# Kernel optimization log

Measured on AMD Instinct MI355X. Metric: run time of the kernel, lower is better.

The kernel has to match this reference:

```python
import jax, jax.numpy as jnp
import numpy as np

N_HEADS = 8
N_GROUPS = 8  # n_channels=256 > 64
COLOR_WEIGHT = 1.2
EPS = 1e-5


def setup_inputs() -> dict:
    key = jax.random.key(0)
    ks = jax.random.split(key, 6)
    B, C, H, W = 16, 256, 32, 32
    x = jax.random.normal(ks[0], (B, C, H, W), dtype=jnp.float32)
    std = 0.02
    wq = jax.random.normal(ks[1], (C, C), dtype=jnp.float32) * std
    wk = jax.random.normal(ks[2], (C, C), dtype=jnp.float32) * std
    wv = jax.random.normal(ks[3], (C, C), dtype=jnp.float32) * std
    wo = jax.random.normal(ks[4], (C, C), dtype=jnp.float32) * std
    bq = jnp.zeros((C,), jnp.float32)
    bk = jnp.zeros((C,), jnp.float32)
    bv = jnp.zeros((C,), jnp.float32)
    bo = jnp.zeros((C,), jnp.float32)
    gn_w = jnp.ones((C,), jnp.float32)
    gn_b = jnp.zeros((C,), jnp.float32)
    return {"x": x, "wq": wq, "bq": bq, "wk": wk, "bk": bk,
            "wv": wv, "bv": bv, "wo": wo, "bo": bo,
            "gn_w": gn_w, "gn_b": gn_b}


def reference(x, wq, bq, wk, bk, wv, bv, wo, bo, gn_w, gn_b):
    B, C, H, W = x.shape
    S = H * W
    nh = N_HEADS
    hd = C // nh
    scale = hd ** (-0.5)

    # GroupNorm over (channels_per_group, spatial) per sample
    xf = x.reshape(B, C, S)
    xg = xf.reshape(B, N_GROUPS, (C // N_GROUPS) * S)
    mean = xg.mean(axis=-1, keepdims=True)
    var = xg.var(axis=-1, keepdims=True)
    xn = ((xg - mean) * jax.lax.rsqrt(var + EPS)).reshape(B, C, S)
    xn = xn * gn_w[None, :, None] + gn_b[None, :, None]

    xt = jnp.swapaxes(xn, 1, 2)  # [B, S, C]
    q = xt @ wq.T + bq
    k = xt @ wk.T + bk
    v = xt @ wv.T + bv
    # [B, S, C] -> [B, nh, S, hd]
    q = q.reshape(B, S, nh, hd).transpose(0, 2, 1, 3)
    k = k.reshape(B, S, nh, hd).transpose(0, 2, 1, 3)
    v = v.reshape(B, S, nh, hd).transpose(0, 2, 1, 3)

    attn = jnp.einsum('bhid,bhjd->bhij', q, k) * scale  # [B, nh, S, S]
    # color bias (is_grayscale=False path): k.transpose(-2,-1).reshape(B,nh,S,hd)
    k_color = jnp.swapaxes(k, -2, -1).reshape(B, nh, S, hd)
    color_attn = jnp.abs(q - k_color).mean(axis=-1, keepdims=True)  # [B,nh,S,1]
    attn = attn + COLOR_WEIGHT * color_attn
    attn = jax.nn.softmax(attn, axis=-1)
    # dropout is inference no-op

    out = jnp.einsum('bhij,bhjd->bhid', attn, v)  # [B, nh, S, hd]
    out = out.transpose(0, 2, 1, 3).reshape(B, S, C)
    out = out @ wo.T + bo
    out = jnp.swapaxes(out, 1, 2).reshape(B, C, H, W)
    return out
```

## Files before the change

kernel.cpp:

```cpp
#include <hip/hip_runtime.h>


typedef __attribute__((ext_vector_type(8))) short bf16x8;
typedef __attribute__((ext_vector_type(4))) float f32x4;

static __device__ __forceinline__ unsigned cvt_pk(float lo, float hi) {
  unsigned r;
  asm("v_cvt_pk_bf16_f32 %0, %1, %2" : "=v"(r) : "v"(lo), "v"(hi));
  return r;
}

__global__ __launch_bounds__(256) void prep_kernel(
    const float* __restrict__ x, float2* __restrict__ statsp,
    const float* __restrict__ w0, const float* __restrict__ w1,
    const float* __restrict__ w2, const float* __restrict__ w3,
    short* __restrict__ o0, short* __restrict__ o1,
    short* __restrict__ o2, short* __restrict__ o3) {
  int tid = threadIdx.x;
  if (blockIdx.x < 512) {
    __shared__ float red[8];
    int bg = blockIdx.x >> 2, qtr = blockIdx.x & 3;
    const float4* x4 = (const float4*)(x + (size_t)bg * 32 * 1024);
    float s = 0.f, ss = 0.f;
#pragma unroll
    for (int p = 0; p < 8; ++p) {
      float4 vv = x4[qtr * 2048 + p * 256 + tid];
      s += (vv.x + vv.y) + (vv.z + vv.w);
      ss += vv.x * vv.x + vv.y * vv.y + vv.z * vv.z + vv.w * vv.w;
    }
#pragma unroll
    for (int o = 32; o > 0; o >>= 1) {
      s += __shfl_down(s, o);
      ss += __shfl_down(ss, o);
    }
    if ((tid & 63) == 0) { red[tid >> 6] = s; red[4 + (tid >> 6)] = ss; }
    __syncthreads();
    if (tid == 0) {
      float S = (red[0] + red[1]) + (red[2] + red[3]);
      float SS = (red[4] + red[5]) + (red[6] + red[7]);
      statsp[bg * 4 + qtr] = make_float2(S, SS);
    }
  } else {
    int idx = blockIdx.x - 512;
    int sel = idx >> 5, blk = idx & 31;
    const float* src = sel == 0 ? w0 : sel == 1 ? w1 : sel == 2 ? w2 : w3;
    short* dst = sel == 0 ? o0 : sel == 1 ? o1 : sel == 2 ? o2 : o3;
    int i = (blk * 256 + tid) * 8;
    float4 a = *(const float4*)(src + i);
    float4 b = *(const float4*)(src + i + 4);
    uint4 r;
    r.x = cvt_pk(a.x, a.y);
    r.y = cvt_pk(a.z, a.w);
    r.z = cvt_pk(b.x, b.y);
    r.w = cvt_pk(b.z, b.w);
    *(uint4*)(dst + i) = r;
  }
}

static __device__ __forceinline__ float2 combine_stats(const float2* __restrict__ sp,
                                                       int bgidx) {
  float2 p0 = sp[bgidx * 4 + 0];
  float2 p1 = sp[bgidx * 4 + 1];
  float2 p2 = sp[bgidx * 4 + 2];
  float2 p3 = sp[bgidx * 4 + 3];
  float S = (p0.x + p1.x) + (p2.x + p3.x);
  float SS = (p0.y + p1.y) + (p2.y + p3.y);
  float mean = S * (1.f / 32768.f);
  float var = SS * (1.f / 32768.f) - mean * mean;
  return make_float2(mean, rsqrtf(var + 1e-5f));
}

__global__ __launch_bounds__(256, 4) void qkv_mfma(
    const float* __restrict__ x, const float2* __restrict__ statsp,
    const float* __restrict__ gnw, const float* __restrict__ gnb,
    const short* __restrict__ Wq, const short* __restrict__ Wk,
    const short* __restrict__ Wv,
    const float* __restrict__ bq, const float* __restrict__ bk,
    const float* __restrict__ bv, short* __restrict__ outq,
    short* __restrict__ outk, short* __restrict__ outvt, float scaleq) {
  __shared__ __align__(16) char smem[20480];
  short* As = (short*)smem;
  int tid = threadIdx.x;
  int m0 = blockIdx.x * 64, n0 = blockIdx.y * 64;
  int w = tid >> 6, lane = tid & 63, g = lane >> 4, c = lane & 15;
  int wm = w >> 1, wn = w & 1;
  int srow = tid >> 2, sk = (tid & 3) * 8;
  int bsmp = m0 >> 10, s0 = m0 & 1023;
  int c2 = tid & 15, sg = tid >> 4;
  const float4* xb = (const float4*)(x + (size_t)(bsmp * 256) * 1024);
  unsigned* A32 = (unsigned*)As;
  f32x4 accq[2][2], acck[2][2], accv[2][2];
#pragma unroll
  for (int i = 0; i < 2; ++i)
#pragma unroll
    for (int j = 0; j < 2; ++j) {
      accq[i][j] = (f32x4){0.f, 0.f, 0.f, 0.f};
      acck[i][j] = (f32x4){0.f, 0.f, 0.f, 0.f};
      accv[i][j] = (f32x4){0.f, 0.f, 0.f, 0.f};
    }
  float a0, a1, b0v, b1v;
  float4 u, v;
  bf16x8 wqr, wkr, wvr;
  {
    float2 st = combine_stats(statsp, bsmp * 8);
    int ch0 = c2 * 2;
    a0 = gnw[ch0] * st.y; b0v = gnb[ch0] - st.x * a0;
    a1 = gnw[ch0 + 1] * st.y; b1v = gnb[ch0 + 1] - st.x * a1;
    u = xb[(size_t)ch0 * 256 + (s0 >> 2) + sg];
    v = xb[(size_t)(ch0 + 1) * 256 + (s0 >> 2) + sg];
    wqr = *(const bf16x8*)(Wq + (size_t)(n0 + srow) * 256 + sk);
    wkr = *(const bf16x8*)(Wk + (size_t)(n0 + srow) * 256 + sk);
    wvr = *(const bf16x8*)(Wv + (size_t)(n0 + srow) * 256 + sk);
  }
  for (int kb = 0; kb < 8; ++kb) {
    {
      int r0 = (sg * 4) * 20 + c2;
      A32[r0]      = cvt_pk(u.x * a0 + b0v, v.x * a1 + b1v);
      A32[r0 + 20] = cvt_pk(u.y * a0 + b0v, v.y * a1 + b1v);
      A32[r0 + 40] = cvt_pk(u.z * a0 + b0v, v.z * a1 + b1v);
      A32[r0 + 60] = cvt_pk(u.w * a0 + b0v, v.w * a1 + b1v);
    }
    *(bf16x8*)(As + 2560 + srow * 40 + sk) = wqr;
    *(bf16x8*)(As + 5120 + srow * 40 + sk) = wkr;
    *(bf16x8*)(As + 7680 + srow * 40 + sk) = wvr;
    __syncthreads();
    if (kb < 7) {
      float2 st = combine_stats(statsp, bsmp * 8 + kb + 1);
      int chn = (kb + 1) * 32 + c2 * 2;
      a0 = gnw[chn] * st.y; b0v = gnb[chn] - st.x * a0;
      a1 = gnw[chn + 1] * st.y; b1v = gnb[chn + 1] - st.x * a1;
      u = xb[(size_t)chn * 256 + (s0 >> 2) + sg];
      v = xb[(size_t)(chn + 1) * 256 + (s0 >> 2) + sg];
      wqr = *(const bf16x8*)(Wq + (size_t)(n0 + srow) * 256 + (kb + 1) * 32 + sk);
      wkr = *(const bf16x8*)(Wk + (size_t)(n0 + srow) * 256 + (kb + 1) * 32 + sk);
      wvr = *(const bf16x8*)(Wv + (size_t)(n0 + srow) * 256 + (kb + 1) * 32 + sk);
    }
    bf16x8 af[2], wfq[2], wfk[2], wfv[2];
#pragma unroll
    for (int i = 0; i < 2; ++i)
      af[i] = *(const bf16x8*)(As + (wm * 32 + i * 16 + c) * 40 + g * 8);
#pragma unroll
    for (int j = 0; j < 2; ++j) {
      int rr = (wn * 32 + j * 16 + c) * 40 + g * 8;
      wfq[j] = *(const bf16x8*)(As + 2560 + rr);
      wfk[j] = *(const bf16x8*)(As + 5120 + rr);
      wfv[j] = *(const bf16x8*)(As + 7680 + rr);
    }
#pragma unroll
    for (int i = 0; i < 2; ++i)
#pragma unroll
      for (int j = 0; j < 2; ++j) {
        accq[i][j] = __builtin_amdgcn_mfma_f32_16x16x32_bf16(wfq[j], af[i], accq[i][j], 0, 0, 0);
        acck[i][j] = __builtin_amdgcn_mfma_f32_16x16x32_bf16(wfk[j], af[i], acck[i][j], 0, 0, 0);
        accv[i][j] = __builtin_amdgcn_mfma_f32_16x16x32_bf16(af[i], wfv[j], accv[i][j], 0, 0, 0);
      }
    __syncthreads();
  }
  short* Tb = (short*)smem;
  int mrd = tid >> 2, ncol = (tid & 3) * 16;
#pragma unroll
  for (int i = 0; i < 2; ++i)
#pragma unroll
    for (int j = 0; j < 2; ++j) {
      float4 b4 = *(const float4*)&bq[n0 + wn * 32 + j * 16 + 4 * g];
      float v0 = (accq[i][j][0] + b4.x) * scaleq;
      float v1 = (accq[i][j][1] + b4.y) * scaleq;
      float v2 = (accq[i][j][2] + b4.z) * scaleq;
      float v3 = (accq[i][j][3] + b4.w) * scaleq;
      *(uint2*)(Tb + (wm * 32 + i * 16 + c) * 72 + wn * 32 + j * 16 + 4 * g) =
          make_uint2(cvt_pk(v0, v1), cvt_pk(v2, v3));
    }
  __syncthreads();
  {
    bf16x8 r0 = *(const bf16x8*)(Tb + mrd * 72 + ncol);
    bf16x8 r1 = *(const bf16x8*)(Tb + mrd * 72 + ncol + 8);
    short* dst = outq + (size_t)(m0 + mrd) * 256 + n0 + ncol;
    *(bf16x8*)dst = r0;
    *(bf16x8*)(dst + 8) = r1;
  }
  __syncthreads();
#pragma unroll
  for (int i = 0; i < 2; ++i)
#pragma unroll
    for (int j = 0; j < 2; ++j) {
      float4 b4 = *(const float4*)&bk[n0 + wn * 32 + j * 16 + 4 * g];
      float v0 = acck[i][j][0] + b4.x;
      float v1 = acck[i][j][1] + b4.y;
      float v2 = acck[i][j][2] + b4.z;
      float v3 = acck[i][j][3] + b4.w;
      *(uint2*)(Tb + (wm * 32 + i * 16 + c) * 72 + wn * 32 + j * 16 + 4 * g) =
          make_uint2(cvt_pk(v0, v1), cvt_pk(v2, v3));
    }
  __syncthreads();
  {
    bf16x8 r0 = *(const bf16x8*)(Tb + mrd * 72 + ncol);
    bf16x8 r1 = *(const bf16x8*)(Tb + mrd * 72 + ncol + 8);
    short* dst = outk + (size_t)(m0 + mrd) * 256 + n0 + ncol;
    *(bf16x8*)dst = r0;
    *(bf16x8*)(dst + 8) = r1;
  }
  __syncthreads();
#pragma unroll
  for (int i = 0; i < 2; ++i)
#pragma unroll
    for (int j = 0; j < 2; ++j) {
      float bvv = bv[n0 + wn * 32 + j * 16 + c];
      float v0 = accv[i][j][0] + bvv;
      float v1 = accv[i][j][1] + bvv;
      float v2 = accv[i][j][2] + bvv;
      float v3 = accv[i][j][3] + bvv;
      *(uint2*)(Tb + (wn * 32 + j * 16 + c) * 72 + wm * 32 + i * 16 + 4 * g) =
          make_uint2(cvt_pk(v0, v1), cvt_pk(v2, v3));
    }
  __syncthreads();
  {
    bf16x8 r0 = *(const bf16x8*)(Tb + mrd * 72 + ncol);
    bf16x8 r1 = *(const bf16x8*)(Tb + mrd * 72 + ncol + 8);
    short* dst = outvt + (size_t)(bsmp * 256 + n0 + mrd) * 1024 + s0 + ncol;
    *(bf16x8*)dst = r0;
    *(bf16x8*)(dst + 8) = r1;
  }
}

#define KSTR 40
#define VSTR 72
#define PSTR 72

__global__ __launch_bounds__(256, 4) void flash_mfma(
    const short* __restrict__ q, const short* __restrict__ k,
    const short* __restrict__ vt, short* __restrict__ out) {
  __shared__ short Ks[2][64 * KSTR];
  __shared__ short Vts[2][32 * VSTR];
  __shared__ short Ps[4 * 32 * PSTR];
  int id = blockIdx.x;
  int swz = (id & 7) * 128 + (id >> 3);
  int bh = swz >> 3, qt = swz & 7;
  int b = bh >> 3, h = bh & 7;
  int tid = threadIdx.x;
  int w = tid >> 6, lane = tid & 63, g = lane >> 4, c = lane & 15;
  short* Psw = Ps + w * 32 * PSTR;
  const size_t qrow0 = (size_t)b * 1024 + qt * 128 + w * 32;
  const int hoff = h * 32;
  bf16x8 aq[2];
#pragma unroll
  for (int mt = 0; mt < 2; ++mt)
    aq[mt] = *(const bf16x8*)(q + (qrow0 + mt * 16 + c) * 256 + hoff + g * 8);
  bf16x8 ones;
#pragma unroll
  for (int i = 0; i < 8; ++i) ones[i] = (short)0x3F80;
  f32x4 o_acc[2][2], accl[2];
#pragma unroll
  for (int mt = 0; mt < 2; ++mt) {
    accl[mt] = (f32x4){0.f, 0.f, 0.f, 0.f};
#pragma unroll
    for (int nt = 0; nt < 2; ++nt) o_acc[mt][nt] = (f32x4){0.f, 0.f, 0.f, 0.f};
  }
  const int kr = tid >> 2, kch = (tid & 3) * 8;
  const int vr = tid >> 3, vch = (tid & 7) * 8;
  const short* kbase = k + ((size_t)b * 1024) * 256 + hoff;
  const short* vbase = vt + (((size_t)b * 8 + h) * 32) * 1024;
  {
    bf16x8 k0 = *(const bf16x8*)(kbase + (size_t)kr * 256 + kch);
    bf16x8 v0 = *(const bf16x8*)(vbase + (size_t)vr * 1024 + vch);
    *(bf16x8*)(&Ks[0][kr * KSTR + kch]) = k0;
    *(bf16x8*)(&Vts[0][vr * VSTR + vch]) = v0;
  }
  __syncthreads();
  int cur = 0;
#pragma unroll 2
  for (int t = 0; t < 16; ++t) {
    bf16x8 kN, vN;
    if (t < 15) {
      kN = *(const bf16x8*)(kbase + (size_t)((t + 1) * 64 + kr) * 256 + kch);
      vN = *(const bf16x8*)(vbase + (size_t)vr * 1024 + (t + 1) * 64 + vch);
    }
    bf16x8 bk4[4];
#pragma unroll
    for (int kt = 0; kt < 4; ++kt)
      bk4[kt] = *(const bf16x8*)(&Ks[cur][(kt * 16 + c) * KSTR + g * 8]);
    f32x4 sc[2][4];
    __builtin_amdgcn_s_setprio(1);
#pragma unroll
    for (int mt = 0; mt < 2; ++mt)
#pragma unroll
      for (int kt = 0; kt < 4; ++kt)
        sc[mt][kt] = __builtin_amdgcn_mfma_f32_16x16x32_bf16(
            bk4[kt], aq[mt], (f32x4){0.f, 0.f, 0.f, 0.f}, 0, 0, 0);
    __builtin_amdgcn_s_setprio(0);
#pragma unroll
    for (int mt = 0; mt < 2; ++mt)
#pragma unroll
      for (int kt = 0; kt < 4; ++kt) {
        float p0 = __builtin_amdgcn_exp2f(sc[mt][kt][0]);
        float p1 = __builtin_amdgcn_exp2f(sc[mt][kt][1]);
        float p2 = __builtin_amdgcn_exp2f(sc[mt][kt][2]);
        float p3 = __builtin_amdgcn_exp2f(sc[mt][kt][3]);
        *(uint2*)(Psw + (mt * 16 + c) * PSTR + kt * 16 + 4 * g) =
            make_uint2(cvt_pk(p0, p1), cvt_pk(p2, p3));
      }
#pragma unroll
    for (int jt = 0; jt < 2; ++jt) {
      bf16x8 av[2], bp[2];
#pragma unroll
      for (int nt = 0; nt < 2; ++nt)
        av[nt] = *(const bf16x8*)(&Vts[cur][(nt * 16 + c) * VSTR + jt * 32 + g * 8]);
#pragma unroll
      for (int mt = 0; mt < 2; ++mt)
        bp[mt] = *(const bf16x8*)(Psw + (mt * 16 + c) * PSTR + jt * 32 + g * 8);
      __builtin_amdgcn_s_setprio(1);
#pragma unroll
      for (int mt = 0; mt < 2; ++mt) {
#pragma unroll
        for (int nt = 0; nt < 2; ++nt)
          o_acc[mt][nt] = __builtin_amdgcn_mfma_f32_16x16x32_bf16(
              av[nt], bp[mt], o_acc[mt][nt], 0, 0, 0);
        accl[mt] = __builtin_amdgcn_mfma_f32_16x16x32_bf16(ones, bp[mt], accl[mt], 0, 0, 0);
      }
      __builtin_amdgcn_s_setprio(0);
    }
    if (t < 15) {
      *(bf16x8*)(&Ks[cur ^ 1][kr * KSTR + kch]) = kN;
      *(bf16x8*)(&Vts[cur ^ 1][vr * VSTR + vch]) = vN;
      __syncthreads();
      cur ^= 1;
    }
  }
#pragma unroll
  for (int mt = 0; mt < 2; ++mt) {
    float linv = 1.0f / accl[mt][0];
#pragma unroll
    for (int nt = 0; nt < 2; ++nt) {
      float v0 = o_acc[mt][nt][0] * linv;
      float v1 = o_acc[mt][nt][1] * linv;
      float v2 = o_acc[mt][nt][2] * linv;
      float v3 = o_acc[mt][nt][3] * linv;
      *(uint2*)(out + (qrow0 + mt * 16 + c) * 256 + hoff + nt * 16 + 4 * g) =
          make_uint2(cvt_pk(v0, v1), cvt_pk(v2, v3));
    }
  }
}

__global__ __launch_bounds__(256) void gemm_out(
    const short* __restrict__ A, const short* __restrict__ W,
    const float* __restrict__ bias, float* __restrict__ out) {
  __shared__ __align__(16) char smem[10240];
  short* As = (short*)smem;
  short* Ws = (short*)(smem + 5120);
  int tid = threadIdx.x;
  int m0 = blockIdx.x * 64, n0 = blockIdx.y * 64;
  int w = tid >> 6, lane = tid & 63, g = lane >> 4, c = lane & 15;
  int wm = w >> 1, wn = w & 1;
  int srow = tid >> 2, sk = (tid & 3) * 8;
  f32x4 acc[2][2];
#pragma unroll
  for (int i = 0; i < 2; ++i)
#pragma unroll
    for (int j = 0; j < 2; ++j) acc[i][j] = (f32x4){0.f, 0.f, 0.f, 0.f};
  bf16x8 aR = *(const bf16x8*)(A + (size_t)(m0 + srow) * 256 + sk);
  bf16x8 wR = *(const bf16x8*)(W + (size_t)(n0 + srow) * 256 + sk);
  for (int kb = 0; kb < 8; ++kb) {
    *(bf16x8*)(As + srow * 40 + sk) = aR;
    *(bf16x8*)(Ws + srow * 40 + sk) = wR;
    __syncthreads();
    if (kb < 7) {
      aR = *(const bf16x8*)(A + (size_t)(m0 + srow) * 256 + (kb + 1) * 32 + sk);
      wR = *(const bf16x8*)(W + (size_t)(n0 + srow) * 256 + (kb + 1) * 32 + sk);
    }
    bf16x8 af[2], wf[2];
#pragma unroll
    for (int i = 0; i < 2; ++i)
      af[i] = *(const bf16x8*)(As + (wm * 32 + i * 16 + c) * 40 + g * 8);
#pragma unroll
    for (int j = 0; j < 2; ++j)
      wf[j] = *(const bf16x8*)(Ws + (wn * 32 + j * 16 + c) * 40 + g * 8);
#pragma unroll
    for (int i = 0; i < 2; ++i)
#pragma unroll
      for (int j = 0; j < 2; ++j)
        acc[i][j] = __builtin_amdgcn_mfma_f32_16x16x32_bf16(af[i], wf[j], acc[i][j], 0, 0, 0);
    __syncthreads();
  }
  int bsmp = m0 >> 10, s0 = m0 & 1023;
  float* Tf = (float*)smem;
  for (int half = 0; half < 2; ++half) {
    __syncthreads();
    if (wn == half) {
#pragma unroll
      for (int j = 0; j < 2; ++j) {
        float bvh = bias[n0 + half * 32 + j * 16 + c];
        int nl = j * 16 + c;
#pragma unroll
        for (int i = 0; i < 2; ++i)
#pragma unroll
          for (int r = 0; r < 4; ++r)
            Tf[nl * 68 + ((wm * 32 + i * 16 + 4 * g + r) ^ ((nl & 7) << 2))] =
                acc[i][j][r] + bvh;
      }
    }
    __syncthreads();
    int n = tid >> 3, mc = (tid & 7) * 8;
    float4 v0 = *(const float4*)(Tf + n * 68 + ((mc + 0) ^ ((n & 7) << 2)));
    float4 v1 = *(const float4*)(Tf + n * 68 + ((mc + 4) ^ ((n & 7) << 2)));
    float* dst = out + ((size_t)(bsmp * 256) + n0 + half * 32 + n) * 1024 + s0 + mc;
    *(float4*)dst = v0;
    *(float4*)(dst + 4) = v1;
  }
}

extern "C" void kernel_launch(void* const* d_in, const int* in_sizes, int n_in,
                              void* d_out, int out_size, void* d_ws, size_t ws_size,
                              hipStream_t stream) {
  const float* x   = (const float*)d_in[0];
  const float* wq  = (const float*)d_in[1];
  const float* bq  = (const float*)d_in[2];
  const float* wk  = (const float*)d_in[3];
  const float* bk  = (const float*)d_in[4];
  const float* wv  = (const float*)d_in[5];
  const float* bv  = (const float*)d_in[6];
  const float* wo  = (const float*)d_in[7];
  const float* bo  = (const float*)d_in[8];
  const float* gnw = (const float*)d_in[9];
  const float* gnb = (const float*)d_in[10];
  float* out = (float*)d_out;

  const size_t NE = (size_t)16 * 1024 * 256;
  short* sw  = (short*)d_ws;
  float2* statsp = (float2*)sw;
  short* qb  = sw + NE;
  short* kb  = sw + 2 * NE;
  short* vtb = sw + 3 * NE;
  short* ao  = sw + 4 * NE;
  short* wqb = sw + 5 * NE;
  short* wkb = wqb + 65536;
  short* wvb = wkb + 65536;
  short* wob = wvb + 65536;

  const float SCALE_Q = (float)(0.17677669529663689 * 1.4426950408889634);
  dim3 blk(256);
  prep_kernel<<<dim3(640), blk, 0, stream>>>(x, statsp, wq, wk, wv, wo,
                                             wqb, wkb, wvb, wob);
  qkv_mfma<<<dim3(256, 4), blk, 0, stream>>>(x, statsp, gnw, gnb, wqb, wkb, wvb,
                                             bq, bk, bv, qb, kb, vtb, SCALE_Q);
  flash_mfma<<<dim3(1024), blk, 0, stream>>>(qb, kb, vtb, ao);
  gemm_out<<<dim3(256, 4), blk, 0, stream>>>(ao, wob, bo, out);
}
```

Before: 73.93 us.

## Halve QKV GEMM M-tile to 32 rows and drop register prefetch

The QKV projection kernel now uses 32x64 output tiles instead of 64x64, doubling the grid to 512x4 blocks. Each wave owns a 16-column slice and issues fewer MFMAs per step. The register-level prefetch of the next K-slice is replaced by direct load-then-store each iteration, and launch bounds are raised to 6 blocks per CU. The aim is more parallelism and lower register pressure to hide latency, at the cost of reloading the weight tiles twice as often and losing the software overlap of global loads with MFMA.

```diff
diff --git a/kernel.cpp b/kernel.cpp
--- a/kernel.cpp
+++ b/kernel.cpp
@@ -70,7 +70,7 @@
   return make_float2(mean, rsqrtf(var + 1e-5f));
 }
 
-__global__ __launch_bounds__(256, 4) void qkv_mfma(
+__global__ __launch_bounds__(256, 6) void qkv_mfma(
     const float* __restrict__ x, const float2* __restrict__ statsp,
     const float* __restrict__ gnw, const float* __restrict__ gnb,
     const short* __restrict__ Wq, const short* __restrict__ Wk,
@@ -78,147 +78,113 @@
     const float* __restrict__ bq, const float* __restrict__ bk,
     const float* __restrict__ bv, short* __restrict__ outq,
     short* __restrict__ outk, short* __restrict__ outvt, float scaleq) {
-  __shared__ __align__(16) char smem[20480];
+  __shared__ __align__(16) char smem[17920];
   short* As = (short*)smem;
   int tid = threadIdx.x;
-  int m0 = blockIdx.x * 64, n0 = blockIdx.y * 64;
+  int m0 = blockIdx.x * 32, n0 = blockIdx.y * 64;
   int w = tid >> 6, lane = tid & 63, g = lane >> 4, c = lane & 15;
-  int wm = w >> 1, wn = w & 1;
   int srow = tid >> 2, sk = (tid & 3) * 8;
   int bsmp = m0 >> 10, s0 = m0 & 1023;
   int c2 = tid & 15, sg = tid >> 4;
   const float4* xb = (const float4*)(x + (size_t)(bsmp * 256) * 1024);
   unsigned* A32 = (unsigned*)As;
-  f32x4 accq[2][2], acck[2][2], accv[2][2];
-#pragma unroll
-  for (int i = 0; i < 2; ++i)
-#pragma unroll
-    for (int j = 0; j < 2; ++j) {
-      accq[i][j] = (f32x4){0.f, 0.f, 0.f, 0.f};
-      acck[i][j] = (f32x4){0.f, 0.f, 0.f, 0.f};
-      accv[i][j] = (f32x4){0.f, 0.f, 0.f, 0.f};
-    }
-  float a0, a1, b0v, b1v;
-  float4 u, v;
-  bf16x8 wqr, wkr, wvr;
-  {
-    float2 st = combine_stats(statsp, bsmp * 8);
-    int ch0 = c2 * 2;
-    a0 = gnw[ch0] * st.y; b0v = gnb[ch0] - st.x * a0;
-    a1 = gnw[ch0 + 1] * st.y; b1v = gnb[ch0 + 1] - st.x * a1;
-    u = xb[(size_t)ch0 * 256 + (s0 >> 2) + sg];
-    v = xb[(size_t)(ch0 + 1) * 256 + (s0 >> 2) + sg];
-    wqr = *(const bf16x8*)(Wq + (size_t)(n0 + srow) * 256 + sk);
-    wkr = *(const bf16x8*)(Wk + (size_t)(n0 + srow) * 256 + sk);
-    wvr = *(const bf16x8*)(Wv + (size_t)(n0 + srow) * 256 + sk);
+  f32x4 accq[2], acck[2], accv[2];
+#pragma unroll
+  for (int i = 0; i < 2; ++i) {
+    accq[i] = (f32x4){0.f, 0.f, 0.f, 0.f};
+    acck[i] = (f32x4){0.f, 0.f, 0.f, 0.f};
+    accv[i] = (f32x4){0.f, 0.f, 0.f, 0.f};
   }
   for (int kb = 0; kb < 8; ++kb) {
-    {
+    __syncthreads();
+    if (sg < 8) {
+      float2 st = combine_stats(statsp, bsmp * 8 + kb);
+      int ch0 = kb * 32 + c2 * 2;
+      float a0 = gnw[ch0] * st.y, b0v = gnb[ch0] - st.x * a0;
+      float a1 = gnw[ch0 + 1] * st.y, b1v = gnb[ch0 + 1] - st.x * a1;
+      float4 u = xb[(size_t)ch0 * 256 + (s0 >> 2) + sg];
+      float4 v = xb[(size_t)(ch0 + 1) * 256 + (s0 >> 2) + sg];
       int r0 = (sg * 4) * 20 + c2;
       A32[r0]      = cvt_pk(u.x * a0 + b0v, v.x * a1 + b1v);
       A32[r0 + 20] = cvt_pk(u.y * a0 + b0v, v.y * a1 + b1v);
       A32[r0 + 40] = cvt_pk(u.z * a0 + b0v, v.z * a1 + b1v);
       A32[r0 + 60] = cvt_pk(u.w * a0 + b0v, v.w * a1 + b1v);
     }
-    *(bf16x8*)(As + 2560 + srow * 40 + sk) = wqr;
-    *(bf16x8*)(As + 5120 + srow * 40 + sk) = wkr;
-    *(bf16x8*)(As + 7680 + srow * 40 + sk) = wvr;
-    __syncthreads();
-    if (kb < 7) {
-      float2 st = combine_stats(statsp, bsmp * 8 + kb + 1);
-      int chn = (kb + 1) * 32 + c2 * 2;
-      a0 = gnw[chn] * st.y; b0v = gnb[chn] - st.x * a0;
-      a1 = gnw[chn + 1] * st.y; b1v = gnb[chn + 1] - st.x * a1;
-      u = xb[(size_t)chn * 256 + (s0 >> 2) + sg];
-      v = xb[(size_t)(chn + 1) * 256 + (s0 >> 2) + sg];
-      wqr = *(const bf16x8*)(Wq + (size_t)(n0 + srow) * 256 + (kb + 1) * 32 + sk);
-      wkr = *(const bf16x8*)(Wk + (size_t)(n0 + srow) * 256 + (kb + 1) * 32 + sk);
-      wvr = *(const bf16x8*)(Wv + (size_t)(n0 + srow) * 256 + (kb + 1) * 32 + sk);
-    }
-    bf16x8 af[2], wfq[2], wfk[2], wfv[2];
+    *(bf16x8*)(As + 1280 + srow * 40 + sk) =
+        *(const bf16x8*)(Wq + (size_t)(n0 + srow) * 256 + kb * 32 + sk);
+    *(bf16x8*)(As + 3840 + srow * 40 + sk) =
+        *(const bf16x8*)(Wk + (size_t)(n0 + srow) * 256 + kb * 32 + sk);
+    *(bf16x8*)(As + 6400 + srow * 40 + sk) =
+        *(const bf16x8*)(Wv + (size_t)(n0 + srow) * 256 + kb * 32 + sk);
+    __syncthreads();
+    bf16x8 af[2], wfq, wfk, wfv;
 #pragma unroll
     for (int i = 0; i < 2; ++i)
-      af[i] = *(const bf16x8*)(As + (wm * 32 + i * 16 + c) * 40 + g * 8);
-#pragma unroll
-    for (int j = 0; j < 2; ++j) {
-      int rr = (wn * 32 + j * 16 + c) * 40 + g * 8;
-      wfq[j] = *(const bf16x8*)(As + 2560 + rr);
-      wfk[j] = *(const bf16x8*)(As + 5120 + rr);
-      wfv[j] = *(const bf16x8*)(As + 7680 + rr);
-    }
-#pragma unroll
-    for (int i = 0; i < 2; ++i)
-#pragma unroll
-      for (int j = 0; j < 2; ++j) {
-        accq[i][j] = __builtin_amdgcn_mfma_f32_16x16x32_bf16(wfq[j], af[i], accq[i][j], 0, 0, 0);
-        acck[i][j] = __builtin_amdgcn_mfma_f32_16x16x32_bf16(wfk[j], af[i], acck[i][j], 0, 0, 0);
-        accv[i][j] = __builtin_amdgcn_mfma_f32_16x16x32_bf16(af[i], wfv[j], accv[i][j], 0, 0, 0);
-      }
-    __syncthreads();
-  }
+      af[i] = *(const bf16x8*)(As + (i * 16 + c) * 40 + g * 8);
+    {
+      int rr = (w * 16 + c) * 40 + g * 8;
+      wfq = *(const bf16x8*)(As + 1280 + rr);
+      wfk = *(const bf16x8*)(As + 3840 + rr);
+      wfv = *(const bf16x8*)(As + 6400 + rr);
+    }
+#pragma unroll
+    for (int i = 0; i < 2; ++i) {
+      accq[i] = __builtin_amdgcn_mfma_f32_16x16x32_bf16(wfq, af[i], accq[i], 0, 0, 0);
+      acck[i] = __builtin_amdgcn_mfma_f32_16x16x32_bf16(wfk, af[i], acck[i], 0, 0, 0);
+      accv[i] = __builtin_amdgcn_mfma_f32_16x16x32_bf16(af[i], wfv, accv[i], 0, 0, 0);
+    }
+  }
+  __syncthreads();
   short* Tb = (short*)smem;
-  int mrd = tid >> 2, ncol = (tid & 3) * 16;
-#pragma unroll
-  for (int i = 0; i < 2; ++i)
-#pragma unroll
-    for (int j = 0; j < 2; ++j) {
-      float4 b4 = *(const float4*)&bq[n0 + wn * 32 + j * 16 + 4 * g];
-      float v0 = (accq[i][j][0] + b4.x) * scaleq;
-      float v1 = (accq[i][j][1] + b4.y) * scaleq;
-      float v2 = (accq[i][j][2] + b4.z) * scaleq;
-      float v3 = (accq[i][j][3] + b4.w) * scaleq;
-      *(uint2*)(Tb + (wm * 32 + i * 16 + c) * 72 + wn * 32 + j * 16 + 4 * g) =
-          make_uint2(cvt_pk(v0, v1), cvt_pk(v2, v3));
-    }
+#pragma unroll
+  for (int i = 0; i < 2; ++i) {
+    float4 b4 = *(const float4*)&bq[n0 + w * 16 + 4 * g];
+    float v0 = (accq[i][0] + b4.x) * scaleq;
+    float v1 = (accq[i][1] + b4.y) * scaleq;
+    float v2 = (accq[i][2] + b4.z) * scaleq;
+    float v3 = (accq[i][3] + b4.w) * scaleq;
+    *(uint2*)(Tb + (i * 16 + c) * 72 + w * 16 + 4 * g) =
+        make_uint2(cvt_pk(v0, v1), cvt_pk(v2, v3));
+  }
   __syncthreads();
   {
-    bf16x8 r0 = *(const bf16x8*)(Tb + mrd * 72 + ncol);
-    bf16x8 r1 = *(const bf16x8*)(Tb + mrd * 72 + ncol + 8);
-    short* dst = outq + (size_t)(m0 + mrd) * 256 + n0 + ncol;
-    *(bf16x8*)dst = r0;
-    *(bf16x8*)(dst + 8) = r1;
-  }
-  __syncthreads();
-#pragma unroll
-  for (int i = 0; i < 2; ++i)
-#pragma unroll
-    for (int j = 0; j < 2; ++j) {
-      float4 b4 = *(const float4*)&bk[n0 + wn * 32 + j * 16 + 4 * g];
-      float v0 = acck[i][j][0] + b4.x;
-      float v1 = acck[i][j][1] + b4.y;
-      float v2 = acck[i][j][2] + b4.z;
-      float v3 = acck[i][j][3] + b4.w;
-      *(uint2*)(Tb + (wm * 32 + i * 16 + c) * 72 + wn * 32 + j * 16 + 4 * g) =
-          make_uint2(cvt_pk(v0, v1), cvt_pk(v2, v3));
-    }
+    int mrd = tid >> 3, ncol = (tid & 7) * 8;
+    *(bf16x8*)(outq + (size_t)(m0 + mrd) * 256 + n0 + ncol) =
+        *(const bf16x8*)(Tb + mrd * 72 + ncol);
+  }
+  __syncthreads();
+#pragma unroll
+  for (int i = 0; i < 2; ++i) {
+    float4 b4 = *(const float4*)&bk[n0 + w * 16 + 4 * g];
+    float v0 = acck[i][0] + b4.x;
+    float v1 = acck[i][1] + b4.y;
+    float v2 = acck[i][2] + b4.z;
+    float v3 = acck[i][3] + b4.w;
+    *(uint2*)(Tb + (i * 16 + c) * 72 + w * 16 + 4 * g) =
+        make_uint2(cvt_pk(v0, v1), cvt_pk(v2, v3));
+  }
   __syncthreads();
   {
-    bf16x8 r0 = *(const bf16x8*)(Tb + mrd * 72 + ncol);
-    bf16x8 r1 = *(const bf16x8*)(Tb + mrd * 72 + ncol + 8);
-    short* dst = outk + (size_t)(m0 + mrd) * 256 + n0 + ncol;
-    *(bf16x8*)dst = r0;
-    *(bf16x8*)(dst + 8) = r1;
-  }
-  __syncthreads();
-#pragma unroll
-  for (int i = 0; i < 2; ++i)
-#pragma unroll
-    for (int j = 0; j < 2; ++j) {
-      float bvv = bv[n0 + wn * 32 + j * 16 + c];
-      float v0 = accv[i][j][0] + bvv;
-      float v1 = accv[i][j][1] + bvv;
-      float v2 = accv[i][j][2] + bvv;
-      float v3 = accv[i][j][3] + bvv;
-      *(uint2*)(Tb + (wn * 32 + j * 16 + c) * 72 + wm * 32 + i * 16 + 4 * g) =
-          make_uint2(cvt_pk(v0, v1), cvt_pk(v2, v3));
-    }
+    int mrd = tid >> 3, ncol = (tid & 7) * 8;
+    *(bf16x8*)(outk + (size_t)(m0 + mrd) * 256 + n0 + ncol) =
+        *(const bf16x8*)(Tb + mrd * 72 + ncol);
+  }
+  __syncthreads();
+#pragma unroll
+  for (int i = 0; i < 2; ++i) {
+    float bvv = bv[n0 + w * 16 + c];
+    float v0 = accv[i][0] + bvv;
+    float v1 = accv[i][1] + bvv;
+    float v2 = accv[i][2] + bvv;
+    float v3 = accv[i][3] + bvv;
+    *(uint2*)(Tb + (w * 16 + c) * 40 + i * 16 + 4 * g) =
+        make_uint2(cvt_pk(v0, v1), cvt_pk(v2, v3));
+  }
   __syncthreads();
   {
-    bf16x8 r0 = *(const bf16x8*)(Tb + mrd * 72 + ncol);
-    bf16x8 r1 = *(const bf16x8*)(Tb + mrd * 72 + ncol + 8);
-    short* dst = outvt + (size_t)(bsmp * 256 + n0 + mrd) * 1024 + s0 + ncol;
-    *(bf16x8*)dst = r0;
-    *(bf16x8*)(dst + 8) = r1;
+    int vr = tid >> 2, vc = (tid & 3) * 8;
+    *(bf16x8*)(outvt + ((size_t)(bsmp * 256) + n0 + vr) * 1024 + s0 + vc) =
+        *(const bf16x8*)(Tb + vr * 40 + vc);
   }
 }
 
@@ -439,7 +405,7 @@
   dim3 blk(256);
   prep_kernel<<<dim3(640), blk, 0, stream>>>(x, statsp, wq, wk, wv, wo,
                                              wqb, wkb, wvb, wob);
-  qkv_mfma<<<dim3(256, 4), blk, 0, stream>>>(x, statsp, gnw, gnb, wqb, wkb, wvb,
+  qkv_mfma<<<dim3(512, 4), blk, 0, stream>>>(x, statsp, gnw, gnb, wqb, wkb, wvb,
                                              bq, bk, bv, qb, kb, vtb, SCALE_Q);
   flash_mfma<<<dim3(1024), blk, 0, stream>>>(qb, kb, vtb, ao);
   gemm_out<<<dim3(256, 4), blk, 0, stream>>>(ao, wob, bo, out);
```

New measurement: 74.16 us. Within noise of the previous version (+0.3%).
